# Optimization experiments

Measured on AMD Instinct MI355X. Metric: run time of the kernel, lower is better.

Reference implementation:

```python
import jax, jax.numpy as jnp
import numpy as np

EMB_DIM = 768
N_WIRES = 10  # (768 - 1).bit_length()
DIM = 2 ** N_WIRES  # 1024
BATCH = 32
SENT_LEN = 128


def _cz_ring_sign(n):
    # Diagonal of (ring of adjacent CZ gates) @ CZ(0, n-1): -1 where an odd
    # number of the qubit pairs (k,k+1) for k<n-1 plus (0,n-1) are both |1>.
    idx = np.arange(2 ** n)
    bits = (idx[:, None] >> (n - 1 - np.arange(n))) & 1  # wire 0 = MSB (kron order)
    par = bits[:, 0] * bits[:, n - 1]
    for k in range(n - 1):
        par = par + bits[:, k] * bits[:, k + 1]
    return jnp.asarray(np.where(par % 2 == 1, -1.0, 1.0).astype(np.complex64))


_CZ_SIGN = _cz_ring_sign(N_WIRES)


def _apply_wire_gates(state, gates):
    # state: (batch, 2**n) complex64; gates: (n, 2, 2) complex64.
    # Contract each 2x2 gate onto its wire instead of building the 2^n x 2^n kron.
    n = gates.shape[0]
    b = state.shape[0]
    v = state.reshape((b,) + (2,) * n)
    for k in range(n):
        v = jnp.moveaxis(v, 1 + k, -1)
        v = v @ gates[k].T  # new_i = sum_j G[i, j] * old_j
        v = jnp.moveaxis(v, -1, 1 + k)
    return v.reshape(b, -1)


def _circuit(s, theta_x, theta_y):
    # [RXLayer, RYLayer, CZRing] repeated 3 times with SHARED parameters
    # (ModuleList([a,b,c]*3) reuses the same module instances).
    cx, sx = jnp.cos(theta_x), jnp.sin(theta_x)
    gx = jnp.stack([jnp.stack([cx, -1j * sx], -1),
                    jnp.stack([-1j * sx, cx], -1)], -2).astype(jnp.complex64)  # (n,2,2)
    cy, sy = jnp.cos(theta_y), jnp.sin(theta_y)
    gy = jnp.stack([jnp.stack([cy, -sy], -1),
                    jnp.stack([sy, cy], -1)], -2).astype(jnp.complex64)  # (n,2,2)
    for _ in range(3):
        s = _apply_wire_gates(s, gx)
        s = _apply_wire_gates(s, gy)
        s = s * _CZ_SIGN  # CZ ring + distant CZ(0, n-1) is diagonal
    return s


def setup_inputs() -> dict:
    key = jax.random.key(0)
    k1, k2, k3 = jax.random.split(key, 3)
    return {
        "x": jax.random.normal(k1, (BATCH, SENT_LEN, EMB_DIM), dtype=jnp.float32),
        "theta_x": jax.random.uniform(k2, (N_WIRES,), dtype=jnp.float32),
        "theta_y": jax.random.uniform(k3, (N_WIRES,), dtype=jnp.float32),
    }


def reference(x, theta_x, theta_y):
    xc = x.astype(jnp.complex64)
    pad = DIM - EMB_DIM
    s = jnp.pad(jnp.mean(xc, axis=1), ((0, 0), (0, pad)))  # (b, 2^n)
    ham = jnp.einsum('bsi,bsj->bij', xc, xc) / xc.shape[1]  # no conj, as in torch
    ham = jnp.pad(ham, ((0, 0), (0, pad), (0, pad)))  # (b, 2^n, 2^n)
    e = _circuit(s, theta_x, theta_y)  # (b, 2^n) complex
    scores = jnp.real(jnp.einsum('bi,bij,bj->b', e, ham, jnp.conj(e)))
    scores = jnp.clip(scores, 0.0, 1.0)
    return scores, e
```

## Files before the change

kernel.cpp:

```cpp
#include <hip/hip_runtime.h>

#define BATCH 32
#define SLEN  128
#define EMB   768
#define DIM   1024
#define NW    10


__global__ void mean_kernel(const float* __restrict__ x, float* __restrict__ m) {
    int eid = blockIdx.x * 256 + threadIdx.x;
    int b = eid / EMB, i = eid % EMB;
    int s0 = blockIdx.y * 32;
    const float* xp = x + (size_t)b * SLEN * EMB + (size_t)s0 * EMB + i;
    float sum = 0.f;
    #pragma unroll 8
    for (int s = 0; s < 32; ++s) sum += xp[(size_t)s * EMB];
    atomicAdd(&m[eid], sum * (1.0f / SLEN));
}

__global__ void __launch_bounds__(512) circuit_kernel(
        const float* __restrict__ m, const float* __restrict__ tx,
        const float* __restrict__ ty, float* __restrict__ e_ws,
        float* __restrict__ e_out, int interleaved) {
    __shared__ float re[DIM], im[DIM];
    __shared__ float cx[NW], sx[NW], cy[NW], sy[NW];
    int b = blockIdx.x, t = threadIdx.x;

    if (t < NW) {
        float a = tx[t]; cx[t] = cosf(a); sx[t] = sinf(a);
        float c = ty[t]; cy[t] = cosf(c); sy[t] = sinf(c);
    }
    for (int i = t; i < DIM; i += 512) {
        re[i] = (i < EMB) ? m[b * EMB + i] : 0.f;
        im[i] = 0.f;
    }
    __syncthreads();

    for (int rep = 0; rep < 3; ++rep) {
        for (int k = 0; k < NW; ++k) {
            int p = 9 - k;
            int i0 = ((t >> p) << (p + 1)) | (t & ((1 << p) - 1));
            int i1 = i0 | (1 << p);
            float c = cx[k], s = sx[k];
            float r0 = re[i0], m0 = im[i0], r1 = re[i1], m1 = im[i1];
            re[i0] = c * r0 + s * m1;  im[i0] = c * m0 - s * r1;
            re[i1] = c * r1 + s * m0;  im[i1] = c * m1 - s * r0;
            __syncthreads();
        }
        for (int k = 0; k < NW; ++k) {
            int p = 9 - k;
            int i0 = ((t >> p) << (p + 1)) | (t & ((1 << p) - 1));
            int i1 = i0 | (1 << p);
            float c = cy[k], s = sy[k];
            float r0 = re[i0], m0 = im[i0], r1 = re[i1], m1 = im[i1];
            re[i0] = c * r0 - s * r1;  im[i0] = c * m0 - s * m1;
            re[i1] = s * r0 + c * r1;  im[i1] = s * m0 + c * m1;
            __syncthreads();
        }
        for (int i = t; i < DIM; i += 512) {
            int par = __popc((i & (i >> 1)) & 0x1FF) + ((i & (i >> 9)) & 1);
            if (par & 1) { re[i] = -re[i]; im[i] = -im[i]; }
        }
        __syncthreads();
    }

    float2* ew = (float2*)e_ws;
    for (int i = t; i < DIM; i += 512) {
        ew[b * DIM + i] = make_float2(re[i], im[i]);
        if (interleaved) {
            ((float2*)e_out)[b * DIM + i] = make_float2(re[i], im[i]);
        } else {
            e_out[b * DIM + i] = re[i];
        }
    }
}

__global__ void score_kernel(const float* __restrict__ x, const float* __restrict__ e_ws,
                             float* __restrict__ acc) {
    __shared__ float uL[EMB], vL[EMB];
    __shared__ float part[4];
    int b = blockIdx.x, chunk = blockIdx.y, t = threadIdx.x;
    const float2* ep = (const float2*)e_ws;
    for (int i = t; i < EMB; i += 256) {
        float2 c = ep[b * DIM + i];
        uL[i] = c.x; vL[i] = c.y;
    }
    __syncthreads();

    int w = t >> 6, l = t & 63;
    float local = 0.f;
    for (int si = 0; si < 4; ++si) {
        int s = chunk * 16 + si * 4 + w;
        const float* xr = x + ((size_t)b * SLEN + s) * EMB;
        float du = 0.f, dv = 0.f;
        #pragma unroll
        for (int j = 0; j < 12; ++j) {
            float xv = xr[l + 64 * j];
            du += xv * uL[l + 64 * j];
            dv += xv * vL[l + 64 * j];
        }
        #pragma unroll
        for (int off = 32; off; off >>= 1) {
            du += __shfl_down(du, off, 64);
            dv += __shfl_down(dv, off, 64);
        }
        if (l == 0) local += du * du + dv * dv;
    }
    if (l == 0) part[w] = local;
    __syncthreads();
    if (t == 0)
        atomicAdd(&acc[b], (part[0] + part[1] + part[2] + part[3]) * (1.0f / SLEN));
}

__global__ void finalize_kernel(const float* __restrict__ acc, float* __restrict__ scores) {
    int b = threadIdx.x;
    if (b < BATCH) scores[b] = fminf(fmaxf(acc[b], 0.f), 1.f);
}

extern "C" void kernel_launch(void* const* d_in, const int* in_sizes, int n_in,
                              void* d_out, int out_size, void* d_ws, size_t ws_size,
                              hipStream_t stream) {
    const float* x  = (const float*)d_in[0];
    const float* tx = (const float*)d_in[1];
    const float* ty = (const float*)d_in[2];
    float* out  = (float*)d_out;
    float* m    = (float*)d_ws;
    float* acc  = m + BATCH * EMB;
    float* e_ws = acc + BATCH;

    int e_elems = out_size - BATCH;
    int interleaved = (e_elems >= BATCH * DIM * 2) ? 1 : 0;

    hipMemsetAsync(d_ws, 0, (BATCH * EMB + BATCH) * sizeof(float), stream);
    mean_kernel<<<dim3(96, 4), 256, 0, stream>>>(x, m);
    circuit_kernel<<<BATCH, 512, 0, stream>>>(m, tx, ty, e_ws, out + BATCH, interleaved);
    score_kernel<<<dim3(BATCH, 8), 256, 0, stream>>>(x, e_ws, acc);
    finalize_kernel<<<1, 64, 0, stream>>>(acc, out);
}
```

Baseline: 86.18 us.

## Fuse mean, circuit, score and finalize into one per-batch kernel

Replaces the memset and four kernel launches with a single 1024-thread block per batch element. Each block computes its own mean, runs the circuit in shared memory, then computes scores directly from shared state, with no workspace round-trips or atomics. This removes launch overhead and global synchronization, but only 32 blocks now stream the 12 MB input twice. That reduces memory-level parallelism compared with the wider grids the separate mean and score kernels used.

```diff
diff --git a/kernel.cpp b/kernel.cpp
--- a/kernel.cpp
+++ b/kernel.cpp
@@ -6,98 +6,86 @@
 #define DIM   1024
 #define NW    10
 
-
-__global__ void mean_kernel(const float* __restrict__ x, float* __restrict__ m) {
-    int eid = blockIdx.x * 256 + threadIdx.x;
-    int b = eid / EMB, i = eid % EMB;
-    int s0 = blockIdx.y * 32;
-    const float* xp = x + (size_t)b * SLEN * EMB + (size_t)s0 * EMB + i;
-    float sum = 0.f;
-    #pragma unroll 8
-    for (int s = 0; s < 32; ++s) sum += xp[(size_t)s * EMB];
-    atomicAdd(&m[eid], sum * (1.0f / SLEN));
-}
-
-__global__ void __launch_bounds__(512) circuit_kernel(
-        const float* __restrict__ m, const float* __restrict__ tx,
-        const float* __restrict__ ty, float* __restrict__ e_ws,
-        float* __restrict__ e_out, int interleaved) {
+__global__ void __launch_bounds__(1024) fused_kernel(
+        const float* __restrict__ x, const float* __restrict__ tx,
+        const float* __restrict__ ty, float* __restrict__ out, int interleaved) {
     __shared__ float re[DIM], im[DIM];
     __shared__ float cx[NW], sx[NW], cy[NW], sy[NW];
+    __shared__ float part[16];
     int b = blockIdx.x, t = threadIdx.x;
 
     if (t < NW) {
         float a = tx[t]; cx[t] = cosf(a); sx[t] = sinf(a);
         float c = ty[t]; cy[t] = cosf(c); sy[t] = sinf(c);
     }
-    for (int i = t; i < DIM; i += 512) {
-        re[i] = (i < EMB) ? m[b * EMB + i] : 0.f;
-        im[i] = 0.f;
+
+    if (t < EMB) {
+        const float* xp = x + (size_t)b * SLEN * EMB + t;
+        float s0 = 0.f, s1 = 0.f, s2 = 0.f, s3 = 0.f;
+        #pragma unroll 8
+        for (int s = 0; s < SLEN; s += 4) {
+            s0 += xp[(size_t)(s + 0) * EMB];
+            s1 += xp[(size_t)(s + 1) * EMB];
+            s2 += xp[(size_t)(s + 2) * EMB];
+            s3 += xp[(size_t)(s + 3) * EMB];
+        }
+        re[t] = (s0 + s1 + s2 + s3) * (1.0f / SLEN);
+    } else {
+        re[t] = 0.f;
     }
+    im[t] = 0.f;
     __syncthreads();
 
     for (int rep = 0; rep < 3; ++rep) {
         for (int k = 0; k < NW; ++k) {
-            int p = 9 - k;
-            int i0 = ((t >> p) << (p + 1)) | (t & ((1 << p) - 1));
-            int i1 = i0 | (1 << p);
-            float c = cx[k], s = sx[k];
-            float r0 = re[i0], m0 = im[i0], r1 = re[i1], m1 = im[i1];
-            re[i0] = c * r0 + s * m1;  im[i0] = c * m0 - s * r1;
-            re[i1] = c * r1 + s * m0;  im[i1] = c * m1 - s * r0;
+            if (t < 512) {
+                int p = 9 - k;
+                int i0 = ((t >> p) << (p + 1)) | (t & ((1 << p) - 1));
+                int i1 = i0 | (1 << p);
+                float c = cx[k], s = sx[k];
+                float r0 = re[i0], m0 = im[i0], r1 = re[i1], m1 = im[i1];
+                re[i0] = c * r0 + s * m1;  im[i0] = c * m0 - s * r1;
+                re[i1] = c * r1 + s * m0;  im[i1] = c * m1 - s * r0;
+            }
             __syncthreads();
         }
         for (int k = 0; k < NW; ++k) {
-            int p = 9 - k;
-            int i0 = ((t >> p) << (p + 1)) | (t & ((1 << p) - 1));
-            int i1 = i0 | (1 << p);
-            float c = cy[k], s = sy[k];
-            float r0 = re[i0], m0 = im[i0], r1 = re[i1], m1 = im[i1];
-            re[i0] = c * r0 - s * r1;  im[i0] = c * m0 - s * m1;
-            re[i1] = s * r0 + c * r1;  im[i1] = s * m0 + c * m1;
+            if (t < 512) {
+                int p = 9 - k;
+                int i0 = ((t >> p) << (p + 1)) | (t & ((1 << p) - 1));
+                int i1 = i0 | (1 << p);
+                float c = cy[k], s = sy[k];
+                float r0 = re[i0], m0 = im[i0], r1 = re[i1], m1 = im[i1];
+                re[i0] = c * r0 - s * r1;  im[i0] = c * m0 - s * m1;
+                re[i1] = s * r0 + c * r1;  im[i1] = s * m0 + c * m1;
+            }
             __syncthreads();
         }
-        for (int i = t; i < DIM; i += 512) {
-            int par = __popc((i & (i >> 1)) & 0x1FF) + ((i & (i >> 9)) & 1);
-            if (par & 1) { re[i] = -re[i]; im[i] = -im[i]; }
+        {
+            int par = __popc((t & (t >> 1)) & 0x1FF) + ((t & (t >> 9)) & 1);
+            if (par & 1) { re[t] = -re[t]; im[t] = -im[t]; }
         }
         __syncthreads();
     }
 
-    float2* ew = (float2*)e_ws;
-    for (int i = t; i < DIM; i += 512) {
-        ew[b * DIM + i] = make_float2(re[i], im[i]);
-        if (interleaved) {
-            ((float2*)e_out)[b * DIM + i] = make_float2(re[i], im[i]);
-        } else {
-            e_out[b * DIM + i] = re[i];
-        }
+    float* e_out = out + BATCH;
+    if (interleaved) {
+        ((float2*)e_out)[b * DIM + t] = make_float2(re[t], im[t]);
+    } else {
+        e_out[b * DIM + t] = re[t];
     }
-}
-
-__global__ void score_kernel(const float* __restrict__ x, const float* __restrict__ e_ws,
-                             float* __restrict__ acc) {
-    __shared__ float uL[EMB], vL[EMB];
-    __shared__ float part[4];
-    int b = blockIdx.x, chunk = blockIdx.y, t = threadIdx.x;
-    const float2* ep = (const float2*)e_ws;
-    for (int i = t; i < EMB; i += 256) {
-        float2 c = ep[b * DIM + i];
-        uL[i] = c.x; vL[i] = c.y;
-    }
-    __syncthreads();
 
     int w = t >> 6, l = t & 63;
     float local = 0.f;
-    for (int si = 0; si < 4; ++si) {
-        int s = chunk * 16 + si * 4 + w;
+    for (int si = 0; si < 8; ++si) {
+        int s = w * 8 + si;
         const float* xr = x + ((size_t)b * SLEN + s) * EMB;
         float du = 0.f, dv = 0.f;
         #pragma unroll
         for (int j = 0; j < 12; ++j) {
             float xv = xr[l + 64 * j];
-            du += xv * uL[l + 64 * j];
-            dv += xv * vL[l + 64 * j];
+            du += xv * re[l + 64 * j];
+            dv += xv * im[l + 64 * j];
         }
         #pragma unroll
         for (int off = 32; off; off >>= 1) {
@@ -108,13 +96,12 @@
     }
     if (l == 0) part[w] = local;
     __syncthreads();
-    if (t == 0)
-        atomicAdd(&acc[b], (part[0] + part[1] + part[2] + part[3]) * (1.0f / SLEN));
-}
-
-__global__ void finalize_kernel(const float* __restrict__ acc, float* __restrict__ scores) {
-    int b = threadIdx.x;
-    if (b < BATCH) scores[b] = fminf(fmaxf(acc[b], 0.f), 1.f);
+    if (t == 0) {
+        float a = 0.f;
+        #pragma unroll
+        for (int i = 0; i < 16; ++i) a += part[i];
+        out[b] = fminf(fmaxf(a * (1.0f / SLEN), 0.f), 1.f);
+    }
 }
 
 extern "C" void kernel_launch(void* const* d_in, const int* in_sizes, int n_in,
@@ -123,17 +110,10 @@
     const float* x  = (const float*)d_in[0];
     const float* tx = (const float*)d_in[1];
     const float* ty = (const float*)d_in[2];
-    float* out  = (float*)d_out;
-    float* m    = (float*)d_ws;
-    float* acc  = m + BATCH * EMB;
-    float* e_ws = acc + BATCH;
+    float* out = (float*)d_out;
 
     int e_elems = out_size - BATCH;
     int interleaved = (e_elems >= BATCH * DIM * 2) ? 1 : 0;
 
-    hipMemsetAsync(d_ws, 0, (BATCH * EMB + BATCH) * sizeof(float), stream);
-    mean_kernel<<<dim3(96, 4), 256, 0, stream>>>(x, m);
-    circuit_kernel<<<BATCH, 512, 0, stream>>>(m, tx, ty, e_ws, out + BATCH, interleaved);
-    score_kernel<<<dim3(BATCH, 8), 256, 0, stream>>>(x, e_ws, acc);
-    finalize_kernel<<<1, 64, 0, stream>>>(acc, out);
+    fused_kernel<<<BATCH, 1024, 0, stream>>>(x, tx, ty, out, interleaved);
 }
```

New measurement: 87.14 us. No clear change (+1.1%).
